# Optimization experiments

Hardware: AMD Instinct MI355X
Metric: run time of the kernel (lower is better)

Reference implementation:

```python
import jax, jax.numpy as jnp
import numpy as np

B, C, H, W = 32, 64, 128, 128
N_KNOTS = 65
GRID = 0.125  # spline_grid_from_range(65, 4.0) = (4.0/32)//1e-6*1e-6 = 0.125


def setup_inputs() -> dict:
    key = jax.random.key(0)
    k1, k2 = jax.random.split(key)
    x = jax.random.normal(k1, (B, C, H, W), dtype=jnp.float32) * 2.0
    coefficients_vect = jax.random.normal(k2, (C * N_KNOTS,), dtype=jnp.float32)
    grid = jnp.float32(GRID)
    zero_knot_indexes = jnp.arange(C, dtype=jnp.int32) * N_KNOTS + N_KNOTS // 2
    return {
        "x": x,
        "coefficients_vect": coefficients_vect,
        "grid": grid,
        "zero_knot_indexes": zero_knot_indexes,
        "size": N_KNOTS,
    }


def reference(x, coefficients_vect, grid, zero_knot_indexes, size):
    half = size // 2
    # clamp so that indexes, indexes+1, indexes+2 stay inside the per-channel table
    x_clamped = jnp.clip(x, -grid * half, grid * (half - 2))
    floored_x = jnp.floor(x_clamped / grid)
    # per-element knot index into flattened (C, n_knots) table
    indexes = (zero_knot_indexes.reshape(1, -1, 1, 1) + floored_x).astype(jnp.int32)
    # fractional position within the knot interval (uses unclamped x, as in torch)
    shift1 = (x - floored_x * grid) / grid
    frac1 = (shift1 - 1) ** 2 / 2
    frac2 = (-2 * shift1**2 + 2 * shift1 + 1) / 2
    frac3 = shift1**2 / 2
    c0 = coefficients_vect[indexes]
    c1 = coefficients_vect[indexes + 1]
    c2 = coefficients_vect[indexes + 2]
    return c2 * frac3 + c1 * frac2 + c0 * frac1
```

## Files before the change

### kernel.cpp

```cpp
#include <hip/hip_runtime.h>


typedef float vfloat4 __attribute__((ext_vector_type(4)));

__device__ __forceinline__ float spline_eval(float xx, const float* lds_c,
                                             float inv_g, float flo, float fhi,
                                             int half) {
    float t   = xx * inv_g;
    float fl  = fminf(fmaxf(floorf(t), flo), fhi);
    int   idx = half + (int)fl;
    float s   = t - fl;
    float u   = s - 1.0f;
    float c0  = lds_c[idx];
    float c1  = lds_c[idx + 1];
    float c2  = lds_c[idx + 2];
    float h0  = 0.5f * (c0 - c1);
    float h2  = 0.5f * (c2 - c1);
    return fmaf(u * u, h0, fmaf(s * s, h2, c1));
}

__global__ __launch_bounds__(256) void quad_spline_kernel(
    const vfloat4* __restrict__ x,
    const float*   __restrict__ coeffs,
    const float*   __restrict__ grid_p,
    const int*     __restrict__ zki,
    const int*     __restrict__ size_p,
    vfloat4*       __restrict__ out)
{
    __shared__ float lds_c[65];

    const int gid = blockIdx.x * 256 + threadIdx.x;
    const int c   = (gid >> 12) & 63;

    const float g    = grid_p[0];
    const int   size = size_p[0];
    const int   half = size >> 1;
    const int   base = zki[c] - half;

    if (threadIdx.x < 65) lds_c[threadIdx.x] = coeffs[base + threadIdx.x];
    __syncthreads();

    const float inv_g = 1.0f / g;
    const float flo   = -(float)half;
    const float fhi   =  (float)(half - 2);

    vfloat4 xv = __builtin_nontemporal_load(&x[gid]);
    vfloat4 r;
    r.x = spline_eval(xv.x, lds_c, inv_g, flo, fhi, half);
    r.y = spline_eval(xv.y, lds_c, inv_g, flo, fhi, half);
    r.z = spline_eval(xv.z, lds_c, inv_g, flo, fhi, half);
    r.w = spline_eval(xv.w, lds_c, inv_g, flo, fhi, half);
    __builtin_nontemporal_store(r, &out[gid]);
}

extern "C" void kernel_launch(void* const* d_in, const int* in_sizes, int n_in,
                              void* d_out, int out_size, void* d_ws, size_t ws_size,
                              hipStream_t stream) {
    const vfloat4* x      = (const vfloat4*)d_in[0];
    const float*   coeffs = (const float*)d_in[1];
    const float*   grid_p = (const float*)d_in[2];
    const int*     zki    = (const int*)d_in[3];
    const int*     size_p = (const int*)d_in[4];
    vfloat4*       out    = (vfloat4*)d_out;

    const int n4     = in_sizes[0] / 4;
    const int blocks = n4 / 256;

    quad_spline_kernel<<<blocks, 256, 0, stream>>>(x, coeffs, grid_p, zki, size_p, out);
}
```

Before: 232.9 us.

## Precompute per-interval polynomial coefficients in LDS and process four vectors per thread

Each block now builds a table of per-interval quadratic coefficients (a0, a1, a2) packed as float4 in LDS, so each element needs one vector LDS read and two FMAs instead of three scalar reads plus extra arithmetic. Each thread handles four float4 vectors, with the global loads issued before the table setup so they overlap the coefficient fetch and barrier. The grid shrinks by 4x, which amortises the per-block setup and sync over more data but lowers the number of blocks available. Evaluating in the power basis may change floating-point rounding slightly.

```diff
diff --git a/kernel.cpp b/kernel.cpp
--- a/kernel.cpp
+++ b/kernel.cpp
@@ -2,22 +2,6 @@
 
 
 typedef float vfloat4 __attribute__((ext_vector_type(4)));
-
-__device__ __forceinline__ float spline_eval(float xx, const float* lds_c,
-                                             float inv_g, float flo, float fhi,
-                                             int half) {
-    float t   = xx * inv_g;
-    float fl  = fminf(fmaxf(floorf(t), flo), fhi);
-    int   idx = half + (int)fl;
-    float s   = t - fl;
-    float u   = s - 1.0f;
-    float c0  = lds_c[idx];
-    float c1  = lds_c[idx + 1];
-    float c2  = lds_c[idx + 2];
-    float h0  = 0.5f * (c0 - c1);
-    float h2  = 0.5f * (c2 - c1);
-    return fmaf(u * u, h0, fmaf(s * s, h2, c1));
-}
 
 __global__ __launch_bounds__(256) void quad_spline_kernel(
     const vfloat4* __restrict__ x,
@@ -27,30 +11,60 @@
     const int*     __restrict__ size_p,
     vfloat4*       __restrict__ out)
 {
-    __shared__ float lds_c[65];
+    __shared__ vfloat4 lds_a[63];
 
-    const int gid = blockIdx.x * 256 + threadIdx.x;
-    const int c   = (gid >> 12) & 63;
+    const int tid   = threadIdx.x;
+    const int vbase = blockIdx.x * 1024 + tid;
+    const int c     = (blockIdx.x >> 2) & 63;
+
+    vfloat4 x0 = __builtin_nontemporal_load(&x[vbase]);
+    vfloat4 x1 = __builtin_nontemporal_load(&x[vbase + 256]);
+    vfloat4 x2 = __builtin_nontemporal_load(&x[vbase + 512]);
+    vfloat4 x3 = __builtin_nontemporal_load(&x[vbase + 768]);
 
     const float g    = grid_p[0];
     const int   size = size_p[0];
     const int   half = size >> 1;
     const int   base = zki[c] - half;
 
-    if (threadIdx.x < 65) lds_c[threadIdx.x] = coeffs[base + threadIdx.x];
+    if (tid < 63) {
+        float c0 = coeffs[base + tid];
+        float c1 = coeffs[base + tid + 1];
+        float c2 = coeffs[base + tid + 2];
+        vfloat4 a;
+        a.x = 0.5f * (c0 + c1);
+        a.y = c1 - c0;
+        a.z = 0.5f * ((c0 - c1) + (c2 - c1));
+        a.w = 0.0f;
+        lds_a[tid] = a;
+    }
     __syncthreads();
 
     const float inv_g = 1.0f / g;
     const float flo   = -(float)half;
     const float fhi   =  (float)(half - 2);
 
-    vfloat4 xv = __builtin_nontemporal_load(&x[gid]);
-    vfloat4 r;
-    r.x = spline_eval(xv.x, lds_c, inv_g, flo, fhi, half);
-    r.y = spline_eval(xv.y, lds_c, inv_g, flo, fhi, half);
-    r.z = spline_eval(xv.z, lds_c, inv_g, flo, fhi, half);
-    r.w = spline_eval(xv.w, lds_c, inv_g, flo, fhi, half);
-    __builtin_nontemporal_store(r, &out[gid]);
+    #define SPLINE(xx, dst)                                            \
+    {                                                                  \
+        float t   = (xx) * inv_g;                                      \
+        float fl  = fminf(fmaxf(floorf(t), flo), fhi);                 \
+        int   idx = half + (int)fl;                                    \
+        float s   = t - fl;                                            \
+        vfloat4 a = lds_a[idx];                                        \
+        (dst) = fmaf(s, fmaf(s, a.z, a.y), a.x);                       \
+    }
+
+    vfloat4 r0, r1, r2, r3;
+    SPLINE(x0.x, r0.x) SPLINE(x0.y, r0.y) SPLINE(x0.z, r0.z) SPLINE(x0.w, r0.w)
+    SPLINE(x1.x, r1.x) SPLINE(x1.y, r1.y) SPLINE(x1.z, r1.z) SPLINE(x1.w, r1.w)
+    SPLINE(x2.x, r2.x) SPLINE(x2.y, r2.y) SPLINE(x2.z, r2.z) SPLINE(x2.w, r2.w)
+    SPLINE(x3.x, r3.x) SPLINE(x3.y, r3.y) SPLINE(x3.z, r3.z) SPLINE(x3.w, r3.w)
+    #undef SPLINE
+
+    __builtin_nontemporal_store(r0, &out[vbase]);
+    __builtin_nontemporal_store(r1, &out[vbase + 256]);
+    __builtin_nontemporal_store(r2, &out[vbase + 512]);
+    __builtin_nontemporal_store(r3, &out[vbase + 768]);
 }
 
 extern "C" void kernel_launch(void* const* d_in, const int* in_sizes, int n_in,
@@ -64,7 +78,7 @@
     vfloat4*       out    = (vfloat4*)d_out;
 
     const int n4     = in_sizes[0] / 4;
-    const int blocks = n4 / 256;
+    const int blocks = n4 / 1024;
 
     quad_spline_kernel<<<blocks, 256, 0, stream>>>(x, coeffs, grid_p, zki, size_p, out);
 }
```

Result: faster. 224.4 us (median of 2 runs) (-3.6%).
